# Performance work log

Hardware: AMD Instinct MI355X
Metric: run time of the kernel (lower is better)

The kernel has to match this reference:

```python
import jax, jax.numpy as jnp
import numpy as np


def setup_inputs() -> dict:
    key = jax.random.key(0)
    k1, k2, k3, k4, k5 = jax.random.split(key, 5)
    B, L, H = 32, 2048, 768
    in1 = jax.random.normal(k1, (B, H), dtype=jnp.float32)
    in2 = jax.random.normal(k2, (B, H), dtype=jnp.float32)
    text = jax.random.normal(k3, (B, L, H), dtype=jnp.float32)
    textmask = jnp.ones((B, L), dtype=jnp.float32)  # 1 = valid token
    # learned params (nn.Linear weights are [out, in]); small scale avoids tanh saturation
    W2 = jax.random.normal(k4, (H, 3 * H), dtype=jnp.float32) * 0.02
    b2 = jnp.zeros((H,), dtype=jnp.float32)
    W1 = jax.random.normal(k5, (1, H), dtype=jnp.float32) * 0.02
    b1 = jnp.zeros((1,), dtype=jnp.float32)
    return {"in1": in1, "in2": in2, "text": text, "textmask": textmask,
            "W2": W2, "b2": b2, "W1": W1, "b1": b1}


def reference(in1, in2, text, textmask, W2, b2, W1, b1):
    H = in1.shape[-1]
    # Split linear2 weight along input dim instead of materializing cat([in1,in2,text]).
    # Same math: cat @ W2.T == in1@W2a.T + in2@W2b.T + text@W2c.T
    W2a, W2b, W2c = W2[:, :H], W2[:, H:2 * H], W2[:, 2 * H:]
    bias_bh = in1 @ W2a.T + in2 @ W2b.T + b2          # [B, H], broadcast over L
    h = jnp.tanh(jnp.einsum('blh,gh->blg', text, W2c) + bias_bh[:, None, :])  # [B, L, H]
    att = jnp.einsum('blh,h->bl', h, W1[0]) + b1[0]   # [B, L]
    att = jax.nn.softmax((1.0 - textmask) * (-1e20) + att, axis=-1)  # masked softmax [B, L]
    context = jnp.einsum('bl,blh->bh', att, text)     # weighted sum [B, H]
    return context, att[:, None, :]                   # matches (context, att[B,1,L])
```

## Files before the change

kernel.cpp:

```cpp
#include <hip/hip_runtime.h>
#include <hip/hip_bf16.h>

typedef __bf16 bf16x8 __attribute__((ext_vector_type(8)));
typedef __bf16 bf16x4 __attribute__((ext_vector_type(4)));
typedef float  f32x4  __attribute__((ext_vector_type(4)));

#define H 768
#define LSEQ 2048
#define BATCH 32
#define MROWS (BATCH*LSEQ)
#define NT 6
#define W2S 2304

__device__ __forceinline__ void gload_lds16(const void* g, void* l){
  __builtin_amdgcn_global_load_lds((const __attribute__((address_space(1))) void*)g,
                                   (__attribute__((address_space(3))) void*)l, 16, 0, 0);
}

__global__ void w2c_cvt_k(const float* __restrict__ W2, __bf16* __restrict__ w2cb){
  int i4 = blockIdx.x*256 + threadIdx.x;
  int g  = i4 / 192;
  int hc = (i4 % 192) * 4;
  f32x4 v = *(const f32x4*)(W2 + (size_t)g*W2S + 1536 + hc);
  bf16x4 o; o[0]=(__bf16)v[0]; o[1]=(__bf16)v[1]; o[2]=(__bf16)v[2]; o[3]=(__bf16)v[3];
  *(bf16x4*)(w2cb + (size_t)g*H + hc) = o;
}

__global__ void bias_k(const float* __restrict__ in1, const float* __restrict__ in2,
                       const float* __restrict__ W2, const float* __restrict__ b2,
                       float* __restrict__ bias){
  int b = blockIdx.y;
  int g = blockIdx.x*64 + (threadIdx.x & 63);
  int q = threadIdx.x >> 6;
  const float* wa = W2 + (size_t)g*W2S + q*192;
  const float* wb = wa + H;
  const float* x1 = in1 + b*H + q*192;
  const float* x2 = in2 + b*H + q*192;
  float acc = 0.f;
  #pragma unroll 8
  for (int h=0; h<192; h+=4){
    f32x4 a4 = *(const f32x4*)(wa+h);
    f32x4 c4 = *(const f32x4*)(x1+h);
    f32x4 b4 = *(const f32x4*)(wb+h);
    f32x4 d4 = *(const f32x4*)(x2+h);
    acc += a4[0]*c4[0]+a4[1]*c4[1]+a4[2]*c4[2]+a4[3]*c4[3];
    acc += b4[0]*d4[0]+b4[1]*d4[1]+b4[2]*d4[2]+b4[3]*d4[3];
  }
  __shared__ float sm[4][64];
  sm[q][threadIdx.x&63] = acc;
  __syncthreads();
  if (q==0){
    float r = sm[0][threadIdx.x]+sm[1][threadIdx.x]+sm[2][threadIdx.x]+sm[3][threadIdx.x] + b2[g];
    bias[(size_t)b*H + g] = r;
  }
}

__global__ __launch_bounds__(256) void fused_gemm_att_k(
    const float* __restrict__ text, const __bf16* __restrict__ w2cb,
    const float* __restrict__ bias, const float* __restrict__ W1,
    float* __restrict__ attp)
{
  __shared__ __align__(16) float  a_lds[2][128*32];
  __shared__ __align__(16) __bf16 b_lds[2][128*32];
  __shared__ float att_lds[2][128];

  int lin = blockIdx.x;
  int sl8 = lin >> 3, xcd = lin & 7;
  int mt  = (sl8/6)*8 + xcd;
  int nt  = sl8 % 6;
  int b   = mt >> 4;
  int m0  = mt << 7;
  int t = threadIdx.x, lane = t & 63, wid = t >> 6;
  int wm = wid >> 1, wn = wid & 1;

  const float*  atile = text + (size_t)m0*H;
  const __bf16* btile = w2cb + (size_t)(nt*128)*H;

  f32x4 acc[4][4];
  #pragma unroll
  for (int mi=0;mi<4;++mi)
    #pragma unroll
    for (int ni=0;ni<4;++ni) acc[mi][ni] = (f32x4){0.f,0.f,0.f,0.f};

  auto stage = [&](int bf, int kk){
    #pragma unroll
    for (int j=0;j<4;++j){
      int slot = wid*4 + j;
      int r  = slot*8 + (lane>>3);
      int cg = (lane&7) ^ (r&7);
      gload_lds16(atile + (size_t)r*H + kk*32 + cg*4, &a_lds[bf][slot*256]);
    }
    #pragma unroll
    for (int j=0;j<2;++j){
      int slot = wid*2 + j;
      int n  = slot*16 + (lane>>2);
      int cs = (lane&3) ^ ((n>>1)&3);
      gload_lds16(btile + (size_t)n*H + kk*32 + cs*8, &b_lds[bf][slot*512]);
    }
  };

  auto compute = [&](int bf){
    bf16x8 af[4], bq[4];
    int cg0 = (lane>>4)*2;
    #pragma unroll
    for (int mi=0;mi<4;++mi){
      int row = wm*64 + mi*16 + (lane&15);
      const float* base = &a_lds[bf][row*32];
      f32x4 lo = *(const f32x4*)(base + ((( cg0   ) ^ (row&7))<<2));
      f32x4 hi = *(const f32x4*)(base + (((cg0+1) ^ (row&7))<<2));
      bf16x8 v;
      v[0]=(__bf16)lo[0]; v[1]=(__bf16)lo[1]; v[2]=(__bf16)lo[2]; v[3]=(__bf16)lo[3];
      v[4]=(__bf16)hi[0]; v[5]=(__bf16)hi[1]; v[6]=(__bf16)hi[2]; v[7]=(__bf16)hi[3];
      af[mi]=v;
    }
    int cs = lane>>4;
    #pragma unroll
    for (int ni=0;ni<4;++ni){
      int n = wn*64 + ni*16 + (lane&15);
      bq[ni] = *(const bf16x8*)&b_lds[bf][n*32 + ((cs ^ ((n>>1)&3))<<3)];
    }
    #pragma unroll
    for (int mi=0;mi<4;++mi)
      #pragma unroll
      for (int ni=0;ni<4;++ni)
        acc[mi][ni] = __builtin_amdgcn_mfma_f32_16x16x32_bf16(af[mi], bq[ni], acc[mi][ni], 0,0,0);
  };

  stage(0, 0);
  __syncthreads();
  #pragma unroll 2
  for (int kk=0; kk<24; ++kk){
    if (kk < 23) stage((kk+1)&1, kk+1);
    compute(kk&1);
    __syncthreads();
  }

  float bb[4], ww[4];
  int gb = nt*128 + wn*64 + (lane&15);
  #pragma unroll
  for (int ni=0;ni<4;++ni){ bb[ni]=bias[(size_t)b*H + gb + ni*16]; ww[ni]=W1[gb + ni*16]; }

  float av[16];
  #pragma unroll
  for (int mi=0;mi<4;++mi)
    #pragma unroll
    for (int r=0;r<4;++r){
      float s = 0.f;
      #pragma unroll
      for (int ni=0;ni<4;++ni){
        float x = acc[mi][ni][r] + bb[ni];
        float e = __expf(2.0f*x);
        s += ww[ni] * ((e-1.0f)/(e+1.0f));
      }
      av[mi*4+r] = s;
    }
  #pragma unroll
  for (int off=1; off<16; off<<=1)
    #pragma unroll
    for (int i=0;i<16;++i) av[i] += __shfl_xor(av[i], off);

  if ((lane&15)==0){
    int mg = (lane>>4)*4;
    #pragma unroll
    for (int mi=0;mi<4;++mi)
      #pragma unroll
      for (int r=0;r<4;++r)
        att_lds[wn][wm*64 + mi*16 + mg + r] = av[mi*4+r];
  }
  __syncthreads();
  if (t < 128) attp[(size_t)nt*MROWS + m0 + t] = att_lds[0][t] + att_lds[1][t];
}

__global__ void softmax_k(const float* __restrict__ attp, const float* __restrict__ tmask,
                          const float* __restrict__ b1, float* __restrict__ att){
  int b = blockIdx.x, t = threadIdx.x;
  int lane = t & 63, wv = t >> 6;
  __shared__ float sl[LSEQ];
  __shared__ float red[4];
  float b1v = b1[0];
  float lmax = -3.0e38f;
  for (int i=t; i<LSEQ; i+=256){
    float v = b1v;
    #pragma unroll
    for (int p=0;p<NT;++p) v += attp[(size_t)p*MROWS + b*LSEQ + i];
    v += (1.0f - tmask[b*LSEQ+i]) * -1.0e20f;
    sl[i] = v;
    lmax = fmaxf(lmax, v);
  }
  #pragma unroll
  for (int off=32; off>=1; off>>=1) lmax = fmaxf(lmax, __shfl_xor(lmax, off));
  if (lane==0) red[wv] = lmax;
  __syncthreads();
  float mx = fmaxf(fmaxf(red[0],red[1]), fmaxf(red[2],red[3]));
  __syncthreads();
  float lsum = 0.f;
  for (int i=t; i<LSEQ; i+=256){
    float e = __expf(sl[i]-mx);
    sl[i] = e;
    lsum += e;
  }
  #pragma unroll
  for (int off=32; off>=1; off>>=1) lsum += __shfl_xor(lsum, off);
  if (lane==0) red[wv] = lsum;
  __syncthreads();
  float inv = 1.0f/(red[0]+red[1]+red[2]+red[3]);
  for (int i=t; i<LSEQ; i+=256) att[(size_t)b*LSEQ+i] = sl[i]*inv;
}

__global__ void ctxpart_k(const float* __restrict__ text, const float* __restrict__ att,
                          float* __restrict__ ctxp){
  int chunk = blockIdx.x, b = blockIdx.y, t = threadIdx.x;
  const float* tp = text + ((size_t)(b*LSEQ + chunk*64))*H + 4*t;
  const float* ap = att + (size_t)b*LSEQ + chunk*64;
  f32x4 acc = {0.f,0.f,0.f,0.f};
  #pragma unroll 4
  for (int l=0;l<64;++l){
    float a = ap[l];
    f32x4 v = *(const f32x4*)(tp + (size_t)l*H);
    acc[0] += a*v[0]; acc[1] += a*v[1]; acc[2] += a*v[2]; acc[3] += a*v[3];
  }
  *(f32x4*)(ctxp + ((size_t)(b*32+chunk))*H + 4*t) = acc;
}

__global__ void ctxred_k(const float* __restrict__ ctxp, float* __restrict__ out){
  int b = blockIdx.x, h = threadIdx.x;
  float s = 0.f;
  #pragma unroll 8
  for (int c=0;c<32;++c) s += ctxp[((size_t)(b*32+c))*H + h];
  out[(size_t)b*H + h] = s;
}

extern "C" void kernel_launch(void* const* d_in, const int* in_sizes, int n_in,
                              void* d_out, int out_size, void* d_ws, size_t ws_size,
                              hipStream_t stream){
  (void)in_sizes; (void)n_in; (void)out_size; (void)ws_size;
  const float* in1   = (const float*)d_in[0];
  const float* in2   = (const float*)d_in[1];
  const float* text  = (const float*)d_in[2];
  const float* tmask = (const float*)d_in[3];
  const float* W2    = (const float*)d_in[4];
  const float* b2    = (const float*)d_in[5];
  const float* W1    = (const float*)d_in[6];
  const float* b1    = (const float*)d_in[7];
  float* out = (float*)d_out;
  char*  ws  = (char*)d_ws;
  __bf16* w2cb = (__bf16*)(ws);
  float* biasb = (float*)(ws + 1179648);
  float* attp  = (float*)(ws + 1277952);
  float* ctxp  = (float*)(ws + 2850816);
  float* att_out = out + BATCH*H;

  w2c_cvt_k      <<<dim3(576),   dim3(256), 0, stream>>>(W2, w2cb);
  bias_k         <<<dim3(12,32), dim3(256), 0, stream>>>(in1, in2, W2, b2, biasb);
  fused_gemm_att_k<<<dim3(3072), dim3(256), 0, stream>>>(text, w2cb, biasb, W1, attp);
  softmax_k      <<<dim3(32),    dim3(256), 0, stream>>>(attp, tmask, b1, att_out);
  ctxpart_k      <<<dim3(32,32), dim3(192), 0, stream>>>(text, att_out, ctxp);
  ctxred_k       <<<dim3(32),    dim3(768), 0, stream>>>(ctxp, out);
}
```

Baseline: 207.1 us.

## Widen GEMM N-tile to 256 and convert text to bf16 once through registers

The fused GEMM+attention kernel now uses 128x256 tiles, so there are 3 N-tiles instead of 6 and the fp32 text matrix is re-read from global memory half as often. Text is loaded into registers and converted to bf16 once before being written to LDS, replacing the direct fp32 global-to-LDS copy and the per-MFMA conversion. The XCD-aware block remapping and the LDS XOR swizzles are dropped. The costs are higher register pressure from 32 accumulators per lane, the launch_bounds occupancy hint of 2, and possible LDS bank conflicts from the unswizzled layout.

```diff
diff --git a/kernel.cpp b/kernel.cpp
--- a/kernel.cpp
+++ b/kernel.cpp
@@ -9,7 +9,7 @@
 #define LSEQ 2048
 #define BATCH 32
 #define MROWS (BATCH*LSEQ)
-#define NT 6
+#define NT 3
 #define W2S 2304
 
 __device__ __forceinline__ void gload_lds16(const void* g, void* l){
@@ -55,90 +55,93 @@
   }
 }
 
-__global__ __launch_bounds__(256) void fused_gemm_att_k(
+__global__ __launch_bounds__(256,2) void fused_gemm_att_k(
     const float* __restrict__ text, const __bf16* __restrict__ w2cb,
     const float* __restrict__ bias, const float* __restrict__ W1,
     float* __restrict__ attp)
 {
-  __shared__ __align__(16) float  a_lds[2][128*32];
-  __shared__ __align__(16) __bf16 b_lds[2][128*32];
+  __shared__ __align__(16) __bf16 a_lds[2][128*32];
+  __shared__ __align__(16) __bf16 b_lds[2][256*32];
   __shared__ float att_lds[2][128];
 
   int lin = blockIdx.x;
-  int sl8 = lin >> 3, xcd = lin & 7;
-  int mt  = (sl8/6)*8 + xcd;
-  int nt  = sl8 % 6;
+  int mt  = lin / 3;
+  int nt  = lin % 3;
   int b   = mt >> 4;
   int m0  = mt << 7;
   int t = threadIdx.x, lane = t & 63, wid = t >> 6;
   int wm = wid >> 1, wn = wid & 1;
 
   const float*  atile = text + (size_t)m0*H;
-  const __bf16* btile = w2cb + (size_t)(nt*128)*H;
-
-  f32x4 acc[4][4];
+  const __bf16* btile = w2cb + (size_t)(nt*256)*H;
+
+  f32x4 acc[4][8];
   #pragma unroll
   for (int mi=0;mi<4;++mi)
     #pragma unroll
-    for (int ni=0;ni<4;++ni) acc[mi][ni] = (f32x4){0.f,0.f,0.f,0.f};
-
-  auto stage = [&](int bf, int kk){
+    for (int ni=0;ni<8;++ni) acc[mi][ni] = (f32x4){0.f,0.f,0.f,0.f};
+
+  int ar = t>>3, ac = (t&7)*4;
+  f32x4 aReg[4];
+
+  auto loadA = [&](int kk){
+    #pragma unroll
+    for (int j=0;j<4;++j)
+      aReg[j] = *(const f32x4*)(atile + (size_t)(ar + j*32)*H + kk*32 + ac);
+  };
+  auto writeA = [&](int bf){
+    #pragma unroll
+    for (int j=0;j<4;++j){
+      bf16x4 o; o[0]=(__bf16)aReg[j][0]; o[1]=(__bf16)aReg[j][1];
+                o[2]=(__bf16)aReg[j][2]; o[3]=(__bf16)aReg[j][3];
+      *(bf16x4*)&a_lds[bf][(ar + j*32)*32 + ac] = o;
+    }
+  };
+  auto stageB = [&](int bf, int kk){
     #pragma unroll
     for (int j=0;j<4;++j){
       int slot = wid*4 + j;
-      int r  = slot*8 + (lane>>3);
-      int cg = (lane&7) ^ (r&7);
-      gload_lds16(atile + (size_t)r*H + kk*32 + cg*4, &a_lds[bf][slot*256]);
-    }
-    #pragma unroll
-    for (int j=0;j<2;++j){
-      int slot = wid*2 + j;
       int n  = slot*16 + (lane>>2);
-      int cs = (lane&3) ^ ((n>>1)&3);
-      gload_lds16(btile + (size_t)n*H + kk*32 + cs*8, &b_lds[bf][slot*512]);
-    }
-  };
-
+      gload_lds16(btile + (size_t)n*H + kk*32 + (lane&3)*8, &b_lds[bf][slot*512]);
+    }
+  };
   auto compute = [&](int bf){
-    bf16x8 af[4], bq[4];
-    int cg0 = (lane>>4)*2;
-    #pragma unroll
-    for (int mi=0;mi<4;++mi){
-      int row = wm*64 + mi*16 + (lane&15);
-      const float* base = &a_lds[bf][row*32];
-      f32x4 lo = *(const f32x4*)(base + ((( cg0   ) ^ (row&7))<<2));
-      f32x4 hi = *(const f32x4*)(base + (((cg0+1) ^ (row&7))<<2));
-      bf16x8 v;
-      v[0]=(__bf16)lo[0]; v[1]=(__bf16)lo[1]; v[2]=(__bf16)lo[2]; v[3]=(__bf16)lo[3];
-      v[4]=(__bf16)hi[0]; v[5]=(__bf16)hi[1]; v[6]=(__bf16)hi[2]; v[7]=(__bf16)hi[3];
-      af[mi]=v;
-    }
-    int cs = lane>>4;
-    #pragma unroll
-    for (int ni=0;ni<4;++ni){
-      int n = wn*64 + ni*16 + (lane&15);
-      bq[ni] = *(const bf16x8*)&b_lds[bf][n*32 + ((cs ^ ((n>>1)&3))<<3)];
-    }
+    bf16x8 af[4];
+    int kq = (lane>>4)*8;
     #pragma unroll
     for (int mi=0;mi<4;++mi)
+      af[mi] = *(const bf16x8*)&a_lds[bf][(wm*64 + mi*16 + (lane&15))*32 + kq];
+    #pragma unroll
+    for (int ni=0;ni<8;++ni){
+      bf16x8 bq = *(const bf16x8*)&b_lds[bf][(wn*128 + ni*16 + (lane&15))*32 + kq];
       #pragma unroll
-      for (int ni=0;ni<4;++ni)
-        acc[mi][ni] = __builtin_amdgcn_mfma_f32_16x16x32_bf16(af[mi], bq[ni], acc[mi][ni], 0,0,0);
-  };
-
-  stage(0, 0);
-  __syncthreads();
+      for (int mi=0;mi<4;++mi)
+        acc[mi][ni] = __builtin_amdgcn_mfma_f32_16x16x32_bf16(af[mi], bq, acc[mi][ni], 0,0,0);
+    }
+  };
+
+  loadA(0);
+  writeA(0);
+  stageB(0, 0);
+  loadA(1);
+  __syncthreads();
+
   #pragma unroll 2
   for (int kk=0; kk<24; ++kk){
-    if (kk < 23) stage((kk+1)&1, kk+1);
+    int nxt = (kk+1)&1;
+    if (kk+1 < 24){
+      stageB(nxt, kk+1);
+      writeA(nxt);
+      if (kk+2 < 24) loadA(kk+2);
+    }
     compute(kk&1);
     __syncthreads();
   }
 
-  float bb[4], ww[4];
-  int gb = nt*128 + wn*64 + (lane&15);
-  #pragma unroll
-  for (int ni=0;ni<4;++ni){ bb[ni]=bias[(size_t)b*H + gb + ni*16]; ww[ni]=W1[gb + ni*16]; }
+  float bb[8], ww[8];
+  int gb = nt*256 + wn*128 + (lane&15);
+  #pragma unroll
+  for (int ni=0;ni<8;++ni){ bb[ni]=bias[(size_t)b*H + gb + ni*16]; ww[ni]=W1[gb + ni*16]; }
 
   float av[16];
   #pragma unroll
@@ -147,7 +150,7 @@
     for (int r=0;r<4;++r){
       float s = 0.f;
       #pragma unroll
-      for (int ni=0;ni<4;++ni){
+      for (int ni=0;ni<8;++ni){
         float x = acc[mi][ni][r] + bb[ni];
         float e = __expf(2.0f*x);
         s += ww[ni] * ((e-1.0f)/(e+1.0f));
@@ -252,7 +255,7 @@
 
   w2c_cvt_k      <<<dim3(576),   dim3(256), 0, stream>>>(W2, w2cb);
   bias_k         <<<dim3(12,32), dim3(256), 0, stream>>>(in1, in2, W2, b2, biasb);
-  fused_gemm_att_k<<<dim3(3072), dim3(256), 0, stream>>>(text, w2cb, biasb, W1, attp);
+  fused_gemm_att_k<<<dim3(1536), dim3(256), 0, stream>>>(text, w2cb, biasb, W1, attp);
   softmax_k      <<<dim3(32),    dim3(256), 0, stream>>>(attp, tmask, b1, att_out);
   ctxpart_k      <<<dim3(32,32), dim3(192), 0, stream>>>(text, att_out, ctxp);
   ctxred_k       <<<dim3(32),    dim3(768), 0, stream>>>(ctxp, out);
```

Result: faster. 198.3 us (-4.3%).

## Load text A-tiles directly to registers and stage B in large K chunks

Applied to the files above, without the earlier changes.

The GEMM main loop no longer stages the fp32 text tile through LDS. Each lane loads its MFMA fragment straight from global memory into registers, software-pipelined two k-steps ahead. The bf16 weight tile is loaded in 256-wide K passes (3 passes, 64KB LDS) instead of a 32-wide double buffer, which cuts barriers per tile. The change also remaps block-to-XCD assignment, sets occupancy to 2, raises MFMA priority and uses a fast reciprocal in tanh. The risks are uncoalesced 32-byte row-strided global loads for A, higher register pressure, and an exposed B-load latency at the start of each pass.

```diff
diff --git a/kernel.cpp b/kernel.cpp
--- a/kernel.cpp
+++ b/kernel.cpp
@@ -55,26 +55,37 @@
   }
 }
 
-__global__ __launch_bounds__(256) void fused_gemm_att_k(
+__global__ __launch_bounds__(256,2) void fused_gemm_att_k(
     const float* __restrict__ text, const __bf16* __restrict__ w2cb,
     const float* __restrict__ bias, const float* __restrict__ W1,
     float* __restrict__ attp)
 {
-  __shared__ __align__(16) float  a_lds[2][128*32];
-  __shared__ __align__(16) __bf16 b_lds[2][128*32];
+  __shared__ __align__(16) __bf16 b_lds[128*256];
   __shared__ float att_lds[2][128];
 
-  int lin = blockIdx.x;
-  int sl8 = lin >> 3, xcd = lin & 7;
-  int mt  = (sl8/6)*8 + xcd;
-  int nt  = sl8 % 6;
+  int bid = blockIdx.x;
+  int lin = (bid & 7)*384 + (bid >> 3);
+  int mt  = lin / 6;
+  int nt  = lin % 6;
+  int m0  = mt << 7;
   int b   = mt >> 4;
-  int m0  = mt << 7;
   int t = threadIdx.x, lane = t & 63, wid = t >> 6;
   int wm = wid >> 1, wn = wid & 1;
-
-  const float*  atile = text + (size_t)m0*H;
-  const __bf16* btile = w2cb + (size_t)(nt*128)*H;
+  int fr = lane & 15, fc = lane >> 4;
+
+  int r0 = t>>5, g0 = t&31;
+  int gs = g0 ^ r0;
+  const __bf16* bstage = w2cb + (size_t)(nt*128 + r0)*H + gs*8;
+  __bf16* bdst = b_lds + t*8;
+
+  const float* aP[4];
+  #pragma unroll
+  for (int i=0;i<4;++i)
+    aP[i] = text + (size_t)(m0 + wm*64 + i*16 + fr)*H + fc*8;
+
+  int bn[4], bnl[4];
+  #pragma unroll
+  for (int i=0;i<4;++i){ int n = wn*64 + i*16 + fr; bn[i]=n*256; bnl[i]=n&7; }
 
   f32x4 acc[4][4];
   #pragma unroll
@@ -82,61 +93,63 @@
     #pragma unroll
     for (int ni=0;ni<4;++ni) acc[mi][ni] = (f32x4){0.f,0.f,0.f,0.f};
 
-  auto stage = [&](int bf, int kk){
-    #pragma unroll
-    for (int j=0;j<4;++j){
-      int slot = wid*4 + j;
-      int r  = slot*8 + (lane>>3);
-      int cg = (lane&7) ^ (r&7);
-      gload_lds16(atile + (size_t)r*H + kk*32 + cg*4, &a_lds[bf][slot*256]);
-    }
-    #pragma unroll
-    for (int j=0;j<2;++j){
-      int slot = wid*2 + j;
-      int n  = slot*16 + (lane>>2);
-      int cs = (lane&3) ^ ((n>>1)&3);
-      gload_lds16(btile + (size_t)n*H + kk*32 + cs*8, &b_lds[bf][slot*512]);
-    }
-  };
-
-  auto compute = [&](int bf){
-    bf16x8 af[4], bq[4];
-    int cg0 = (lane>>4)*2;
-    #pragma unroll
-    for (int mi=0;mi<4;++mi){
-      int row = wm*64 + mi*16 + (lane&15);
-      const float* base = &a_lds[bf][row*32];
-      f32x4 lo = *(const f32x4*)(base + ((( cg0   ) ^ (row&7))<<2));
-      f32x4 hi = *(const f32x4*)(base + (((cg0+1) ^ (row&7))<<2));
-      bf16x8 v;
-      v[0]=(__bf16)lo[0]; v[1]=(__bf16)lo[1]; v[2]=(__bf16)lo[2]; v[3]=(__bf16)lo[3];
-      v[4]=(__bf16)hi[0]; v[5]=(__bf16)hi[1]; v[6]=(__bf16)hi[2]; v[7]=(__bf16)hi[3];
-      af[mi]=v;
-    }
-    int cs = lane>>4;
-    #pragma unroll
-    for (int ni=0;ni<4;++ni){
-      int n = wn*64 + ni*16 + (lane&15);
-      bq[ni] = *(const bf16x8*)&b_lds[bf][n*32 + ((cs ^ ((n>>1)&3))<<3)];
-    }
-    #pragma unroll
-    for (int mi=0;mi<4;++mi)
-      #pragma unroll
-      for (int ni=0;ni<4;++ni)
-        acc[mi][ni] = __builtin_amdgcn_mfma_f32_16x16x32_bf16(af[mi], bq[ni], acc[mi][ni], 0,0,0);
-  };
-
-  stage(0, 0);
-  __syncthreads();
-  #pragma unroll 2
-  for (int kk=0; kk<24; ++kk){
-    if (kk < 23) stage((kk+1)&1, kk+1);
-    compute(kk&1);
-    __syncthreads();
+  f32x4 ap0[8], ap1[8];
+
+  #pragma unroll 1
+  for (int pass=0; pass<3; ++pass){
+    int kb = pass*256;
+    #pragma unroll
+    for (int i=0;i<4;++i){
+      ap0[2*i]   = *(const f32x4*)(aP[i] + kb);
+      ap0[2*i+1] = *(const f32x4*)(aP[i] + kb + 4);
+    }
+    #pragma unroll
+    for (int i=0;i<4;++i){
+      ap1[2*i]   = *(const f32x4*)(aP[i] + kb + 32);
+      ap1[2*i+1] = *(const f32x4*)(aP[i] + kb + 36);
+    }
+    #pragma unroll
+    for (int j=0;j<16;++j)
+      gload_lds16(bstage + kb + j*(8*H), bdst + j*2048);
+    asm volatile("s_waitcnt vmcnt(0)" ::: "memory");
+    __builtin_amdgcn_s_barrier();
+
+    #pragma unroll
+    for (int ss=0; ss<8; ++ss){
+      f32x4* cur = (ss&1) ? ap1 : ap0;
+      bf16x8 af[4];
+      #pragma unroll
+      for (int i=0;i<4;++i){
+        f32x4 lo = cur[2*i], hi = cur[2*i+1];
+        bf16x8 v;
+        v[0]=(__bf16)lo[0]; v[1]=(__bf16)lo[1]; v[2]=(__bf16)lo[2]; v[3]=(__bf16)lo[3];
+        v[4]=(__bf16)hi[0]; v[5]=(__bf16)hi[1]; v[6]=(__bf16)hi[2]; v[7]=(__bf16)hi[3];
+        af[i]=v;
+      }
+      if (ss < 6){
+        #pragma unroll
+        for (int i=0;i<4;++i){
+          cur[2*i]   = *(const f32x4*)(aP[i] + kb + (ss+2)*32);
+          cur[2*i+1] = *(const f32x4*)(aP[i] + kb + (ss+2)*32 + 4);
+        }
+      }
+      bf16x8 bq[4];
+      #pragma unroll
+      for (int i=0;i<4;++i)
+        bq[i] = *(const bf16x8*)&b_lds[bn[i] + (((ss*4+fc)^bnl[i])<<3)];
+      __builtin_amdgcn_s_setprio(1);
+      #pragma unroll
+      for (int mi=0;mi<4;++mi)
+        #pragma unroll
+        for (int ni=0;ni<4;++ni)
+          acc[mi][ni] = __builtin_amdgcn_mfma_f32_16x16x32_bf16(af[mi], bq[ni], acc[mi][ni], 0,0,0);
+      __builtin_amdgcn_s_setprio(0);
+    }
+    __builtin_amdgcn_s_barrier();
   }
 
   float bb[4], ww[4];
-  int gb = nt*128 + wn*64 + (lane&15);
+  int gb = nt*128 + wn*64 + fr;
   #pragma unroll
   for (int ni=0;ni<4;++ni){ bb[ni]=bias[(size_t)b*H + gb + ni*16]; ww[ni]=W1[gb + ni*16]; }
 
@@ -150,7 +163,7 @@
       for (int ni=0;ni<4;++ni){
         float x = acc[mi][ni][r] + bb[ni];
         float e = __expf(2.0f*x);
-        s += ww[ni] * ((e-1.0f)/(e+1.0f));
+        s += ww[ni] * ((e-1.0f)*__builtin_amdgcn_rcpf(e+1.0f));
       }
       av[mi*4+r] = s;
     }
@@ -159,13 +172,12 @@
     #pragma unroll
     for (int i=0;i<16;++i) av[i] += __shfl_xor(av[i], off);
 
-  if ((lane&15)==0){
-    int mg = (lane>>4)*4;
+  if (fr==0){
     #pragma unroll
     for (int mi=0;mi<4;++mi)
       #pragma unroll
       for (int r=0;r<4;++r)
-        att_lds[wn][wm*64 + mi*16 + mg + r] = av[mi*4+r];
+        att_lds[wn][wm*64 + mi*16 + fc*4 + r] = av[mi*4+r];
   }
   __syncthreads();
   if (t < 128) attp[(size_t)nt*MROWS + m0 + t] = att_lds[0][t] + att_lds[1][t];
```

Measured after the change: 363.5 us. 1.76x slower.
